# Kernel optimization log

Measured on AMD Instinct MI355X. Metric: run time of the kernel, lower is better.

## Reference

```python
import jax, jax.numpy as jnp
import numpy as np
import math

CTX_LEN = 2048
N_EMB = 256
HEAD_SIZE = 256
N_HEADS = 8
HEAD_DIM = HEAD_SIZE // N_HEADS  # 32
B, T = 4, 2048


def setup_inputs() -> dict:
    key = jax.random.key(0)
    k1, k2, k3, k4 = jax.random.split(key, 4)
    x = jax.random.normal(k1, (B, T, N_EMB), dtype=jnp.float32)
    # torch Linear(n_emb, 3*head_size, bias=False): store as [in, out] for x @ W
    w_attn = jax.random.normal(k2, (N_EMB, 3 * HEAD_SIZE), dtype=jnp.float32) * 0.02
    pos_embs = jax.random.normal(k3, (N_HEADS, CTX_LEN, HEAD_DIM), dtype=jnp.float32) * 0.02
    w_proj = jax.random.normal(k4, (HEAD_SIZE, N_EMB), dtype=jnp.float32) * 0.02
    b_proj = jnp.zeros((N_EMB,), dtype=jnp.float32)
    return {"x": x, "w_attn": w_attn, "pos_embs": pos_embs,
            "w_proj": w_proj, "b_proj": b_proj}


def reference(x, w_attn, pos_embs, w_proj, b_proj):
    Bsz, Tlen, _ = x.shape
    qkv = x @ w_attn                               # [B,T,3*HS]
    K, Q, V = jnp.split(qkv, 3, axis=-1)           # split order: K, Q, V (as in source)
    def heads(t):                                  # [B,T,HS] -> [B,H,T,hd]
        return t.reshape(Bsz, Tlen, N_HEADS, HEAD_DIM).transpose(0, 2, 1, 3)
    K, Q, V = heads(K), heads(Q), heads(V)

    # relative position term with skew trick
    pe = pos_embs[:, -Tlen:, :]                    # [H,T,hd]
    S_rel = jnp.einsum('bhtd,hsd->bhts', Q, pe)    # [B,H,T,T]
    flip_mask = jnp.flip(jnp.tril(jnp.ones((Tlen, Tlen), dtype=x.dtype)), axis=1)
    S_rel = S_rel * flip_mask
    # pad a zero column at the front, reshape [T+1,T], drop first row -> skew
    S_rel = jnp.pad(S_rel, ((0, 0), (0, 0), (0, 0), (1, 0)))
    S_rel = S_rel.reshape(Bsz, N_HEADS, Tlen + 1, Tlen)[:, :, 1:, :]

    scores = (jnp.einsum('bhtd,bhsd->bhts', Q, K) + S_rel) / math.sqrt(HEAD_DIM)
    causal = jnp.where(jnp.tril(jnp.ones((Tlen, Tlen), dtype=bool)), 0.0, -1e9).astype(x.dtype)
    scores = scores + causal
    attn = jax.nn.softmax(scores, axis=-1)         # dropout omitted (eval mode)

    out = jnp.einsum('bhts,bhsd->bhtd', attn, V)   # [B,H,T,hd]
    out = out.transpose(0, 2, 1, 3).reshape(Bsz, Tlen, HEAD_SIZE)
    return out @ w_proj + b_proj
```

## Files before the change

### kernel.cpp

```cpp
#include <hip/hip_runtime.h>
#include <math.h>

#define BB 4
#define TT 2048
#define NEMB 256
#define NH 8
#define HD 32

typedef __attribute__((ext_vector_type(8))) short bf8;
typedef __attribute__((ext_vector_type(4))) float f4;

static __device__ __forceinline__ unsigned short f2bf(float f) {
    union { float f; unsigned u; } v; v.f = f;
    unsigned r = v.u + 0x7FFF + ((v.u >> 16) & 1);
    return (unsigned short)(r >> 16);
}

template <int CTRL>
static __device__ __forceinline__ float dppmv(float x) {
    return __int_as_float(__builtin_amdgcn_mov_dpp(__float_as_int(x), CTRL, 0xF, 0xF, true));
}
static __device__ __forceinline__ float rowmax16(float x) {
    x = fmaxf(x, dppmv<0xB1>(x));
    x = fmaxf(x, dppmv<0x4E>(x));
    x = fmaxf(x, dppmv<0x124>(x));
    x = fmaxf(x, dppmv<0x128>(x));
    return x;
}
static __device__ __forceinline__ float rowsum16(float x) {
    x += dppmv<0xB1>(x);
    x += dppmv<0x4E>(x);
    x += dppmv<0x124>(x);
    x += dppmv<0x128>(x);
    return x;
}

static __device__ __forceinline__ void tcvt_body(const float* __restrict__ src,
                                                 unsigned short* __restrict__ dst,
                                                 int R, int C, int gx, int gy,
                                                 float (*t)[65], int tid) {
    const int c0 = gx * 64, r0 = gy * 64;
    #pragma unroll
    for (int p = 0; p < 4; ++p) {
        const int i = tid + p * 256;
        const int r = i >> 4, c4 = (i & 15) * 4;
        const float4 v = *(const float4*)(src + (long)(r0 + r) * C + c0 + c4);
        t[r][c4] = v.x; t[r][c4+1] = v.y; t[r][c4+2] = v.z; t[r][c4+3] = v.w;
    }
    __syncthreads();
    #pragma unroll
    for (int p = 0; p < 4; ++p) {
        const int i = tid + p * 256;
        const int cr = i >> 4, r4 = (i & 15) * 4;
        ushort4 vv;
        vv.x = f2bf(t[r4+0][cr]); vv.y = f2bf(t[r4+1][cr]);
        vv.z = f2bf(t[r4+2][cr]); vv.w = f2bf(t[r4+3][cr]);
        *(ushort4*)(dst + (long)(c0 + cr) * R + r0 + r4) = vv;
    }
}

__global__ __launch_bounds__(256) void prep(const float* __restrict__ x,
                                            unsigned short* __restrict__ xb,
                                            const float* __restrict__ pe,
                                            unsigned short* __restrict__ peb,
                                            const float* __restrict__ wa,
                                            unsigned short* __restrict__ waT,
                                            const float* __restrict__ wp,
                                            unsigned short* __restrict__ wpT) {
    __shared__ float t[64][65];
    const int bx = blockIdx.x, tid = threadIdx.x;
    if (bx < 2048) {
        const long i = (long)bx * 256 + tid;
        const float4 v = ((const float4*)x)[i];
        ushort4 o; o.x = f2bf(v.x); o.y = f2bf(v.y); o.z = f2bf(v.z); o.w = f2bf(v.w);
        ((ushort4*)xb)[i] = o;
    } else if (bx < 2560) {
        const long i = (long)(bx - 2048) * 256 + tid;
        const float4 v = ((const float4*)pe)[i];
        ushort4 o; o.x = f2bf(v.x); o.y = f2bf(v.y); o.z = f2bf(v.z); o.w = f2bf(v.w);
        ((ushort4*)peb)[i] = o;
    } else if (bx < 2608) {
        const int lo = bx - 2560;
        tcvt_body(wa, waT, 256, 768, lo % 12, lo / 12, t, tid);
    } else {
        const int lo = bx - 2608;
        tcvt_body(wp, wpT, 256, 256, lo % 4, lo / 4, t, tid);
    }
}

__global__ __launch_bounds__(256) void qkv_mfma(const unsigned short* __restrict__ Ag,
                                                const unsigned short* __restrict__ Bg,
                                                unsigned short* __restrict__ Kb,
                                                unsigned short* __restrict__ Qb,
                                                unsigned short* __restrict__ Vt) {
    __shared__ unsigned short sm[13824];
    unsigned short* As = sm;
    unsigned short* Bs = sm + 9216;
    const int tid = threadIdx.x;
    const int wv = tid >> 6, L = tid & 63;
    const int l15 = L & 15, q = L >> 4;
    const int n0 = blockIdx.x * 64;
    const int m0 = blockIdx.y * 128;

    f4 acc[2][4];
    #pragma unroll
    for (int mt = 0; mt < 2; ++mt)
        #pragma unroll
        for (int nt = 0; nt < 4; ++nt) acc[mt][nt] = (f4){0.f,0.f,0.f,0.f};

    for (int kc = 0; kc < 4; ++kc) {
        const int k0 = kc * 64;
        __syncthreads();
        #pragma unroll
        for (int p = 0; p < 4; ++p) {
            const int i = tid + p * 256;
            const int r = i >> 3, c = i & 7;
            *(bf8*)(As + r * 72 + c * 8) = *(const bf8*)(Ag + (long)(m0 + r) * 256 + k0 + c * 8);
        }
        #pragma unroll
        for (int p = 0; p < 2; ++p) {
            const int i = tid + p * 256;
            const int r = i >> 3, c = i & 7;
            *(bf8*)(Bs + r * 72 + c * 8) = *(const bf8*)(Bg + (long)(n0 + r) * 256 + k0 + c * 8);
        }
        __syncthreads();
        #pragma unroll
        for (int kk = 0; kk < 2; ++kk) {
            const bf8 a0 = *(const bf8*)(As + (wv * 32 + l15) * 72 + kk * 32 + q * 8);
            const bf8 a1 = *(const bf8*)(As + (wv * 32 + 16 + l15) * 72 + kk * 32 + q * 8);
            #pragma unroll
            for (int nt = 0; nt < 4; ++nt) {
                const bf8 bb = *(const bf8*)(Bs + (nt * 16 + l15) * 72 + kk * 32 + q * 8);
                acc[0][nt] = __builtin_amdgcn_mfma_f32_16x16x32_bf16(a0, bb, acc[0][nt], 0, 0, 0);
                acc[1][nt] = __builtin_amdgcn_mfma_f32_16x16x32_bf16(a1, bb, acc[1][nt], 0, 0, 0);
            }
        }
    }

    const int sec = n0 >> 8;
    #pragma unroll
    for (int mt = 0; mt < 2; ++mt) {
        const int gm = m0 + wv * 32 + mt * 16 + q * 4;
        const int b = gm >> 11, tb = gm & 2047;
        #pragma unroll
        for (int nt = 0; nt < 4; ++nt) {
            const int gn = n0 + nt * 16 + l15;
            const int cc = gn & 255, h = cc >> 5, d = cc & 31;
            const long bh = (long)b * NH + h;
            const f4 a = acc[mt][nt];
            if (sec == 2) {
                ushort4 vv;
                vv.x = f2bf(a[0]); vv.y = f2bf(a[1]); vv.z = f2bf(a[2]); vv.w = f2bf(a[3]);
                *(ushort4*)(Vt + (bh * HD + d) * TT + tb) = vv;
            } else if (sec == 1) {
                #pragma unroll
                for (int r = 0; r < 4; ++r)
                    Qb[(bh * TT + tb + r) * HD + d] = f2bf(a[r] * 0.25506655788696527f);
            } else {
                #pragma unroll
                for (int r = 0; r < 4; ++r)
                    Kb[(bh * TT + tb + r) * HD + d] = f2bf(a[r]);
            }
        }
    }
}

__global__ __launch_bounds__(256) void attn_kernel(const unsigned short* __restrict__ Kb,
                                                   const unsigned short* __restrict__ Qb,
                                                   const unsigned short* __restrict__ Vtg,
                                                   const unsigned short* __restrict__ peb,
                                                   unsigned short* __restrict__ att) {
    __shared__ unsigned short lds[14592];
    unsigned short* Ks  = lds;
    unsigned short* PEs = lds + 2560;
    unsigned short* Vts = lds + 7680;
    unsigned short* Psw = lds + 9984 + (threadIdx.x >> 6) * 1152;

    const int tid = threadIdx.x;
    const int wv  = tid >> 6;
    const int L   = tid & 63;
    const int l15 = L & 15;
    const int q   = L >> 4;
    const int h = blockIdx.y, b = blockIdx.z;
    const long bh = (long)b * NH + h;
    const unsigned short* Kg = Kb  + bh * TT * HD;
    const unsigned short* Qg = Qb  + bh * TT * HD;
    const unsigned short* Vg = Vtg + bh * HD * TT;
    const unsigned short* Pg = peb + (long)h * TT * HD;

    const int krow = tid >> 2, kc = tid & 3;
    const int vrow = tid >> 3, vc = tid & 7;
    const f4 z4 = {0.f, 0.f, 0.f, 0.f};

    for (int half = 0; half < 2; ++half) {
        const int itile = half ? 31 - (int)blockIdx.x : (int)blockIdx.x;
        const int t0 = itile * 64;

        const bf8 aq = *(const bf8*)(Qg + (t0 + wv * 16 + l15) * HD + q * 8);
        f4 o0 = z4, o1 = z4;
        float m_st[4] = {-1e30f, -1e30f, -1e30f, -1e30f};
        float l_st[4] = {0.f, 0.f, 0.f, 0.f};

        for (int jt = 0; jt <= itile; ++jt) {
            const int s0 = jt * 64;
            const int ubase = TT - 64 - t0 + s0;
            __syncthreads();
            *(bf8*)(Ks  + krow * 40 + kc * 8) = *(const bf8*)(Kg + (s0 + krow) * HD + kc * 8);
            *(bf8*)(Vts + vrow * 72 + vc * 8) = *(const bf8*)(Vg + vrow * TT + s0 + vc * 8);
            #pragma unroll
            for (int kk = 0; kk < 2; ++kk) {
                const int i  = tid + kk * 256;
                const int pr = i >> 2, pc = i & 3;
                const int u  = ubase + pr;
                bf8 val = {0,0,0,0,0,0,0,0};
                if (u < TT) val = *(const bf8*)(Pg + (long)u * HD + pc * 8);
                *(bf8*)(PEs + pr * 40 + pc * 8) = val;
            }
            __syncthreads();

            f4 sa[4], ra[5];
            #pragma unroll
            for (int nt = 0; nt < 4; ++nt) {
                const bf8 bk = *(const bf8*)(Ks + (nt * 16 + l15) * 40 + q * 8);
                sa[nt] = __builtin_amdgcn_mfma_f32_16x16x32_bf16(aq, bk, z4, 0, 0, 0);
            }
            const int pebase = 48 - 16 * wv;
            #pragma unroll
            for (int nt = 0; nt < 5; ++nt) {
                const bf8 bp = *(const bf8*)(PEs + (pebase + nt * 16 + l15) * 40 + q * 8);
                ra[nt] = __builtin_amdgcn_mfma_f32_16x16x32_bf16(aq, bp, z4, 0, 0, 0);
            }

            unsigned short rb[5][4];
            #pragma unroll
            for (int nt = 0; nt < 5; ++nt)
                #pragma unroll
                for (int r = 0; r < 4; ++r) rb[nt][r] = f2bf(ra[nt][r]);
            #pragma unroll
            for (int nb = 0; nb < 4; ++nb) {
                #pragma unroll
                for (int r = 0; r < 4; ++r) {
                    const unsigned packed = (unsigned)rb[nb][r] | ((unsigned)rb[nb + 1][r] << 16);
                    const int shift = 15 - 4 * q - r;
                    const int tcol  = l15 + shift;
                    const int src   = (q << 4) | (tcol & 15);
                    const unsigned v = (unsigned)__shfl((int)packed, src);
                    const unsigned sel = (tcol < 16) ? (v << 16) : (v & 0xFFFF0000u);
                    sa[nb][r] += __int_as_float((int)sel);
                }
            }

            if (jt == itile) {
                #pragma unroll
                for (int nb = 0; nb < 4; ++nb)
                    #pragma unroll
                    for (int r = 0; r < 4; ++r) {
                        const int s_l = nb * 16 + l15;
                        const int t_l = wv * 16 + 4 * q + r;
                        if (s_l > t_l) sa[nb][r] = -1e30f;
                    }
            }

            float corr[4];
            #pragma unroll
            for (int r = 0; r < 4; ++r) {
                float mx = fmaxf(fmaxf(sa[0][r], sa[1][r]), fmaxf(sa[2][r], sa[3][r]));
                mx = rowmax16(mx);
                const float mn = fmaxf(m_st[r], mx);
                corr[r] = exp2f(m_st[r] - mn);
                m_st[r] = mn;
                float rs = 0.f;
                #pragma unroll
                for (int nb = 0; nb < 4; ++nb) {
                    const float p = exp2f(sa[nb][r] - mn);
                    rs += p;
                    Psw[(4 * q + r) * 72 + nb * 16 + l15] = f2bf(p);
                }
                rs = rowsum16(rs);
                l_st[r] = l_st[r] * corr[r] + rs;
            }
            #pragma unroll
            for (int r = 0; r < 4; ++r) { o0[r] *= corr[r]; o1[r] *= corr[r]; }

            #pragma unroll
            for (int ks = 0; ks < 2; ++ks) {
                const bf8 ap  = *(const bf8*)(Psw + l15 * 72 + ks * 32 + q * 8);
                const bf8 bv0 = *(const bf8*)(Vts + l15 * 72 + ks * 32 + q * 8);
                const bf8 bv1 = *(const bf8*)(Vts + (16 + l15) * 72 + ks * 32 + q * 8);
                o0 = __builtin_amdgcn_mfma_f32_16x16x32_bf16(ap, bv0, o0, 0, 0, 0);
                o1 = __builtin_amdgcn_mfma_f32_16x16x32_bf16(ap, bv1, o1, 0, 0, 0);
            }
        }

        #pragma unroll
        for (int r = 0; r < 4; ++r) {
            const float inv = 1.0f / l_st[r];
            const int t = t0 + wv * 16 + 4 * q + r;
            unsigned short* dst = att + ((long)(b * TT + t)) * NEMB + h * HD;
            dst[l15]      = f2bf(o0[r] * inv);
            dst[16 + l15] = f2bf(o1[r] * inv);
        }
    }
}

__global__ __launch_bounds__(256) void proj_mfma(const unsigned short* __restrict__ Ag,
                                                 const unsigned short* __restrict__ Bg,
                                                 const float* __restrict__ bias,
                                                 float* __restrict__ out) {
    __shared__ unsigned short sm[13824];
    unsigned short* As = sm;
    unsigned short* Bs = sm + 9216;
    const int tid = threadIdx.x;
    const int wv = tid >> 6, L = tid & 63;
    const int l15 = L & 15, q = L >> 4;
    const int n0 = blockIdx.x * 64;
    const int m0 = blockIdx.y * 128;

    f4 acc[2][4];
    #pragma unroll
    for (int mt = 0; mt < 2; ++mt)
        #pragma unroll
        for (int nt = 0; nt < 4; ++nt) acc[mt][nt] = (f4){0.f,0.f,0.f,0.f};

    for (int kc = 0; kc < 4; ++kc) {
        const int k0 = kc * 64;
        __syncthreads();
        #pragma unroll
        for (int p = 0; p < 4; ++p) {
            const int i = tid + p * 256;
            const int r = i >> 3, c = i & 7;
            *(bf8*)(As + r * 72 + c * 8) = *(const bf8*)(Ag + (long)(m0 + r) * 256 + k0 + c * 8);
        }
        #pragma unroll
        for (int p = 0; p < 2; ++p) {
            const int i = tid + p * 256;
            const int r = i >> 3, c = i & 7;
            *(bf8*)(Bs + r * 72 + c * 8) = *(const bf8*)(Bg + (long)(n0 + r) * 256 + k0 + c * 8);
        }
        __syncthreads();
        #pragma unroll
        for (int kk = 0; kk < 2; ++kk) {
            const bf8 a0 = *(const bf8*)(As + (wv * 32 + l15) * 72 + kk * 32 + q * 8);
            const bf8 a1 = *(const bf8*)(As + (wv * 32 + 16 + l15) * 72 + kk * 32 + q * 8);
            #pragma unroll
            for (int nt = 0; nt < 4; ++nt) {
                const bf8 bb = *(const bf8*)(Bs + (nt * 16 + l15) * 72 + kk * 32 + q * 8);
                acc[0][nt] = __builtin_amdgcn_mfma_f32_16x16x32_bf16(a0, bb, acc[0][nt], 0, 0, 0);
                acc[1][nt] = __builtin_amdgcn_mfma_f32_16x16x32_bf16(a1, bb, acc[1][nt], 0, 0, 0);
            }
        }
    }

    #pragma unroll
    for (int mt = 0; mt < 2; ++mt) {
        const int gm = m0 + wv * 32 + mt * 16 + q * 4;
        #pragma unroll
        for (int nt = 0; nt < 4; ++nt) {
            const int gn = n0 + nt * 16 + l15;
            const float bv = bias[gn];
            #pragma unroll
            for (int r = 0; r < 4; ++r)
                out[(long)(gm + r) * NEMB + gn] = acc[mt][nt][r] + bv;
        }
    }
}

extern "C" void kernel_launch(void* const* d_in, const int* in_sizes, int n_in,
                              void* d_out, int out_size, void* d_ws, size_t ws_size,
                              hipStream_t stream) {
    const float* x      = (const float*)d_in[0];
    const float* w_attn = (const float*)d_in[1];
    const float* pe     = (const float*)d_in[2];
    const float* w_proj = (const float*)d_in[3];
    const float* b_proj = (const float*)d_in[4];
    float* out = (float*)d_out;

    char* base = (char*)d_ws;
    unsigned short* xb   = (unsigned short*)(base);
    unsigned short* Kb   = (unsigned short*)(base + ( 4u << 20));
    unsigned short* Qb   = (unsigned short*)(base + ( 8u << 20));
    unsigned short* Vt   = (unsigned short*)(base + (12u << 20));
    unsigned short* attb = (unsigned short*)(base + (16u << 20));
    unsigned short* peb  = (unsigned short*)(base + (20u << 20));
    unsigned short* waT  = (unsigned short*)(base + (21u << 20));
    unsigned short* wpT  = (unsigned short*)(base + (22u << 20));

    prep<<<dim3(2624), 256, 0, stream>>>(x, xb, pe, peb, w_attn, waT, w_proj, wpT);
    qkv_mfma<<<dim3(12, 64), 256, 0, stream>>>(xb, waT, Kb, Qb, Vt);
    attn_kernel<<<dim3(16, NH, BB), 256, 0, stream>>>(Kb, Qb, Vt, peb, attb);
    proj_mfma<<<dim3(4, 64), 256, 0, stream>>>(attb, wpT, b_proj, out);
}
```

Measured before the change: 169.1 us.

## Split attention KV range across two blocks and merge partials

Each query-tile pair is now handled by two blocks that take alternating key tiles, which doubles the attention grid from 512 to 1024 blocks. Each block writes a normalized bf16 partial output plus its row max and row sum, and a new merge kernel combines the two partials with log-sum-exp weights before the projection. This is meant to raise occupancy across the GPU's compute units. The cost is an extra kernel launch, extra global traffic for the partials, and a second bf16 rounding of the output.

```diff
diff --git a/kernel.cpp b/kernel.cpp
--- a/kernel.cpp
+++ b/kernel.cpp
@@ -14,6 +14,10 @@
     union { float f; unsigned u; } v; v.f = f;
     unsigned r = v.u + 0x7FFF + ((v.u >> 16) & 1);
     return (unsigned short)(r >> 16);
+}
+static __device__ __forceinline__ float bf2f(unsigned short s) {
+    union { unsigned u; float f; } v; v.u = ((unsigned)s) << 16;
+    return v.f;
 }
 
 template <int CTRL>
@@ -169,7 +173,9 @@
                                                    const unsigned short* __restrict__ Qb,
                                                    const unsigned short* __restrict__ Vtg,
                                                    const unsigned short* __restrict__ peb,
-                                                   unsigned short* __restrict__ att) {
+                                                   unsigned short* __restrict__ po,
+                                                   float* __restrict__ pm,
+                                                   float* __restrict__ pl) {
     __shared__ unsigned short lds[14592];
     unsigned short* Ks  = lds;
     unsigned short* PEs = lds + 2560;
@@ -181,6 +187,8 @@
     const int L   = tid & 63;
     const int l15 = L & 15;
     const int q   = L >> 4;
+    const int pair = blockIdx.x >> 1;
+    const int sblk = blockIdx.x & 1;
     const int h = blockIdx.y, b = blockIdx.z;
     const long bh = (long)b * NH + h;
     const unsigned short* Kg = Kb  + bh * TT * HD;
@@ -193,7 +201,7 @@
     const f4 z4 = {0.f, 0.f, 0.f, 0.f};
 
     for (int half = 0; half < 2; ++half) {
-        const int itile = half ? 31 - (int)blockIdx.x : (int)blockIdx.x;
+        const int itile = half ? 31 - pair : pair;
         const int t0 = itile * 64;
 
         const bf8 aq = *(const bf8*)(Qg + (t0 + wv * 16 + l15) * HD + q * 8);
@@ -201,7 +209,7 @@
         float m_st[4] = {-1e30f, -1e30f, -1e30f, -1e30f};
         float l_st[4] = {0.f, 0.f, 0.f, 0.f};
 
-        for (int jt = 0; jt <= itile; ++jt) {
+        for (int jt = sblk; jt <= itile; jt += 2) {
             const int s0 = jt * 64;
             const int ubase = TT - 64 - t0 + s0;
             __syncthreads();
@@ -292,15 +300,48 @@
             }
         }
 
+        const long pt = (bh * 32 + itile) * 2 + sblk;
+        unsigned short* pob = po + pt * 2048;
         #pragma unroll
         for (int r = 0; r < 4; ++r) {
-            const float inv = 1.0f / l_st[r];
-            const int t = t0 + wv * 16 + 4 * q + r;
-            unsigned short* dst = att + ((long)(b * TT + t)) * NEMB + h * HD;
-            dst[l15]      = f2bf(o0[r] * inv);
-            dst[16 + l15] = f2bf(o1[r] * inv);
-        }
-    }
+            const float inv = (l_st[r] > 0.f) ? (1.0f / l_st[r]) : 0.f;
+            const int row = wv * 16 + 4 * q + r;
+            pob[row * 32 + l15]      = f2bf(o0[r] * inv);
+            pob[row * 32 + 16 + l15] = f2bf(o1[r] * inv);
+            if (l15 == 0) {
+                pm[pt * 64 + row] = m_st[r];
+                pl[pt * 64 + row] = l_st[r];
+            }
+        }
+    }
+}
+
+__global__ __launch_bounds__(256) void attn_merge(const unsigned short* __restrict__ po,
+                                                  const float* __restrict__ pm,
+                                                  const float* __restrict__ pl,
+                                                  unsigned short* __restrict__ attb) {
+    const int i = blockIdx.x * 256 + threadIdx.x;
+    const int d4   = i & 7;
+    const int row  = (i >> 3) & 63;
+    const int tile = (i >> 9) & 31;
+    const int bh   = i >> 14;
+    const int h = bh & 7, b = bh >> 3;
+    const long pt0 = ((long)bh * 32 + tile) * 2;
+    const float m0 = pm[pt0 * 64 + row], m1 = pm[(pt0 + 1) * 64 + row];
+    const float l0 = pl[pt0 * 64 + row], l1 = pl[(pt0 + 1) * 64 + row];
+    const float M  = fmaxf(m0, m1);
+    const float w0 = exp2f(m0 - M) * l0;
+    const float w1 = exp2f(m1 - M) * l1;
+    const float inv = 1.0f / (w0 + w1);
+    const ushort4 a = *(const ushort4*)(po + pt0 * 2048 + row * 32 + d4 * 4);
+    const ushort4 c = *(const ushort4*)(po + (pt0 + 1) * 2048 + row * 32 + d4 * 4);
+    ushort4 o;
+    o.x = f2bf((w0 * bf2f(a.x) + w1 * bf2f(c.x)) * inv);
+    o.y = f2bf((w0 * bf2f(a.y) + w1 * bf2f(c.y)) * inv);
+    o.z = f2bf((w0 * bf2f(a.z) + w1 * bf2f(c.z)) * inv);
+    o.w = f2bf((w0 * bf2f(a.w) + w1 * bf2f(c.w)) * inv);
+    const int t = tile * 64 + row;
+    *(ushort4*)(attb + ((long)(b * TT + t)) * NEMB + h * HD + d4 * 4) = o;
 }
 
 __global__ __launch_bounds__(256) void proj_mfma(const unsigned short* __restrict__ Ag,
@@ -383,10 +424,14 @@
     unsigned short* attb = (unsigned short*)(base + (16u << 20));
     unsigned short* peb  = (unsigned short*)(base + (20u << 20));
     unsigned short* waT  = (unsigned short*)(base + (21u << 20));
-    unsigned short* wpT  = (unsigned short*)(base + (22u << 20));
+    unsigned short* wpT  = (unsigned short*)(base + (43u << 19));
+    unsigned short* po   = (unsigned short*)(base + (22u << 20));
+    float*          pm   = (float*)        (base + (30u << 20));
+    float*          pl   = (float*)        (base + (61u << 19));
 
     prep<<<dim3(2624), 256, 0, stream>>>(x, xb, pe, peb, w_attn, waT, w_proj, wpT);
     qkv_mfma<<<dim3(12, 64), 256, 0, stream>>>(xb, waT, Kb, Qb, Vt);
-    attn_kernel<<<dim3(16, NH, BB), 256, 0, stream>>>(Kb, Qb, Vt, peb, attb);
+    attn_kernel<<<dim3(32, NH, BB), 256, 0, stream>>>(Kb, Qb, Vt, peb, po, pm, pl);
+    attn_merge<<<dim3(2048), 256, 0, stream>>>(po, pm, pl, attb);
     proj_mfma<<<dim3(4, 64), 256, 0, stream>>>(attb, wpT, b_proj, out);
 }
```

Measured after the change: 170.3 us. No clear change (+0.7%).
